# Kernel tuning notes

Hardware: AMD Instinct MI355X
Metric: run time of the kernel (lower is better)

The kernel has to match this reference:

```python
import jax, jax.numpy as jnp
import numpy as np
import math

B, S, D, H, DFF, E, TOPK = 2, 2048, 768, 12, 3072, 8, 2
DH = D // H
EPS = 1e-5


def _ln(x, g, b):
    mu = jnp.mean(x, axis=-1, keepdims=True)
    var = jnp.mean(jnp.square(x - mu), axis=-1, keepdims=True)
    return (x - mu) * jax.lax.rsqrt(var + EPS) * g + b


def _router(x, rw, rb):
    # x: [B,S,D] -> probs [B,S,E], topk indices [B,S,K]
    logits = jnp.einsum('bsd,de->bse', x, rw) + rb
    probs = jax.nn.softmax(logits, axis=-1)
    topv, topi = jax.lax.top_k(probs, TOPK)
    return probs, topv, topi


def setup_inputs() -> dict:
    key = jax.random.key(0)
    ks = jax.random.split(key, 12)
    s = 0.02
    inp = {
        'x': jax.random.normal(ks[0], (B, S, D), dtype=jnp.float32),
        'wq': jax.random.normal(ks[1], (D, D), dtype=jnp.float32) * s,
        'bq': jnp.zeros((D,), jnp.float32),
        'wk': jax.random.normal(ks[2], (D, D), dtype=jnp.float32) * s,
        'bk': jnp.zeros((D,), jnp.float32),
        'wv': jax.random.normal(ks[3], (D, D), dtype=jnp.float32) * s,
        'bv': jnp.zeros((D,), jnp.float32),
        'wo': jax.random.normal(ks[4], (D, D), dtype=jnp.float32) * s,
        'bo': jnp.zeros((D,), jnp.float32),
        'norm1_g': jnp.ones((D,), jnp.float32),
        'norm1_b': jnp.zeros((D,), jnp.float32),
        'router_w': jax.random.normal(ks[5], (D, E), dtype=jnp.float32) * s,
        'router_b': jnp.zeros((E,), jnp.float32),
        'ew1': jax.random.normal(ks[6], (E, D, DFF), dtype=jnp.float32) * s,
        'eb1': jnp.zeros((E, DFF), jnp.float32),
        'ew2': jax.random.normal(ks[7], (E, DFF, D), dtype=jnp.float32) * s,
        'eb2': jnp.zeros((E, D), jnp.float32),
        'norm2_g': jnp.ones((D,), jnp.float32),
        'norm2_b': jnp.zeros((D,), jnp.float32),
    }
    return inp


def reference(x, wq, bq, wk, bk, wv, bv, wo, bo,
              norm1_g, norm1_b, router_w, router_b,
              ew1, eb1, ew2, eb2, norm2_g, norm2_b):
    # ---- multi-head self-attention ----
    def proj(w, b):
        return (jnp.einsum('bsd,de->bse', x, w) + b).reshape(B, S, H, DH).transpose(0, 2, 1, 3)
    q, k, v = proj(wq, bq), proj(wk, bk), proj(wv, bv)
    scores = jnp.einsum('bhqd,bhkd->bhqk', q, k) / math.sqrt(DH)
    attn = jax.nn.softmax(scores, axis=-1)
    ctx = jnp.einsum('bhqk,bhkd->bhqd', attn, v).transpose(0, 2, 1, 3).reshape(B, S, D)
    attn_out = jnp.einsum('bsd,de->bse', ctx, wo) + bo
    x1 = _ln(x + attn_out, norm1_g, norm1_b)

    # ---- MoE: top-k routing with renormalized gates ----
    probs, topv, topi = _router(x1, router_w, router_b)
    gates = topv / jnp.sum(topv, axis=-1, keepdims=True)          # [B,S,K]
    # combine weights per expert: [B,S,E]
    combine = jnp.sum(jax.nn.one_hot(topi, E, dtype=x1.dtype) * gates[..., None], axis=-2)
    moe_out = jnp.zeros_like(x1)
    for e in range(E):  # fixed small expert count
        h = jax.nn.relu(jnp.einsum('bsd,df->bsf', x1, ew1[e]) + eb1[e])
        y = jnp.einsum('bsf,fd->bsd', h, ew2[e]) + eb2[e]
        moe_out = moe_out + combine[..., e:e + 1] * y
    x2 = _ln(x1 + moe_out, norm2_g, norm2_b)

    # ---- redundant second router call + load-balancing aux loss ----
    probs2, _, topi2 = _router(x2, router_w, router_b)
    mask2 = jax.nn.one_hot(topi2, E, dtype=x2.dtype)              # [B,S,K,E]
    frac = jnp.mean(mask2, axis=(0, 1, 2))                        # fraction routed per expert
    prob = jnp.mean(probs2, axis=(0, 1))                          # mean router prob per expert
    aux_loss = E * jnp.sum(frac * prob)
    return (x2, aux_loss)
```

## Files before the change

kernel.cpp:

```cpp
#include <hip/hip_runtime.h>

typedef _Float16 f16;
typedef _Float16 f16x8 __attribute__((ext_vector_type(8)));
typedef _Float16 f16x4v __attribute__((ext_vector_type(4)));
typedef float f32x4 __attribute__((ext_vector_type(4)));

#define THREADS 256
#define BM 128
#define BN 128
#define BKK 64

#define WSCALE 256.0f
#define WDESCALE (1.0f/256.0f)

static __device__ __forceinline__ float wred_sum(float x){
#pragma unroll
  for (int o = 32; o; o >>= 1) x += __shfl_xor(x, o);
  return x;
}
static __device__ __forceinline__ int wred_sumi(int x){
#pragma unroll
  for (int o = 32; o; o >>= 1) x += __shfl_xor(x, o);
  return x;
}
static __device__ __forceinline__ float bred_sum(float x){
  __shared__ float r[4];
  x = wred_sum(x);
  if ((threadIdx.x & 63) == 0) r[threadIdx.x >> 6] = x;
  __syncthreads();
  float s = r[0] + r[1] + r[2] + r[3];
  __syncthreads();
  return s;
}

template<class Epi>
static __device__ __forceinline__ void gemm_core(const f16* A, const f16* BT,
                                                 int m0, int K, int N, int n0, Epi epi)
{
  __shared__ __align__(16) f16 Al[BM][BKK];
  __shared__ __align__(16) f16 Bl[BN][BKK];
  const int t = threadIdx.x;
  const int lane = t & 63, wave = t >> 6;
  const int wr = wave >> 1, wc = wave & 1;

  const f16* gA[4];
  const f16* gB[4];
#pragma unroll
  for (int i = 0; i < 4; ++i) {
    int c = i * THREADS + t;
    int r = c >> 3;
    int kc = (((c & 7) ^ (r & 7)) << 3);
    gA[i] = A + (size_t)(m0 + r) * K + kc;
    gB[i] = BT + (size_t)(n0 + r) * K + kc;
  }

  f32x4 acc[4][4];
#pragma unroll
  for (int i = 0; i < 4; ++i)
#pragma unroll
    for (int j = 0; j < 4; ++j)
#pragma unroll
      for (int r = 0; r < 4; ++r) acc[i][j][r] = 0.0f;

  f16* Als = &Al[0][0];
  f16* Bls = &Bl[0][0];

  for (int k0 = 0; k0 < K; k0 += BKK) {
    __syncthreads();
#pragma unroll
    for (int i = 0; i < 4; ++i) {
      int c = i * THREADS + t;
      __builtin_amdgcn_global_load_lds(
          (const __attribute__((address_space(1))) void*)(gA[i] + k0),
          (__attribute__((address_space(3))) void*)(Als + (size_t)c * 8), 16, 0, 0);
      __builtin_amdgcn_global_load_lds(
          (const __attribute__((address_space(1))) void*)(gB[i] + k0),
          (__attribute__((address_space(3))) void*)(Bls + (size_t)c * 8), 16, 0, 0);
    }
    __syncthreads();
#pragma unroll
    for (int kk = 0; kk < BKK; kk += 32) {
      const int lrow = lane & 15, lk = (lane >> 4) * 8;
      const int sx = (lrow & 7) << 3;
      f16x8 af[4], bf[4];
#pragma unroll
      for (int mf = 0; mf < 4; ++mf)
        af[mf] = *(const f16x8*)&Als[(size_t)(wr * 64 + mf * 16 + lrow) * BKK + ((kk + lk) ^ sx)];
#pragma unroll
      for (int nf = 0; nf < 4; ++nf)
        bf[nf] = *(const f16x8*)&Bls[(size_t)(wc * 64 + nf * 16 + lrow) * BKK + ((kk + lk) ^ sx)];
#pragma unroll
      for (int mf = 0; mf < 4; ++mf)
#pragma unroll
        for (int nf = 0; nf < 4; ++nf)
          acc[mf][nf] = __builtin_amdgcn_mfma_f32_16x16x32_f16(af[mf], bf[nf], acc[mf][nf], 0, 0, 0);
    }
  }
  const int lr4 = (lane >> 4) * 4, lc = lane & 15;
#pragma unroll
  for (int mf = 0; mf < 4; ++mf)
#pragma unroll
    for (int nf = 0; nf < 4; ++nf)
#pragma unroll
      for (int r = 0; r < 4; ++r) {
        int row = wr * 64 + mf * 16 + lr4 + r;
        int col = n0 + wc * 64 + nf * 16 + lc;
        epi(row, col, acc[mf][nf][r]);
      }
}

__global__ __launch_bounds__(256) void k_cvt(const float* x, f16* o){
  size_t i = (size_t)blockIdx.x * 256 + threadIdx.x;
  float4 v = ((const float4*)x)[i];
  f16x4v h;
  h[0] = (f16)v.x; h[1] = (f16)v.y; h[2] = (f16)v.z; h[3] = (f16)v.w;
  *(f16x4v*)(o + i * 4) = h;
}

__global__ __launch_bounds__(256) void k_transpose(const float* in, f16* out, int Kd, int Nd){
  __shared__ float tl[32][33];
  const float* ip = in + (size_t)blockIdx.z * Kd * Nd;
  f16* op = out + (size_t)blockIdx.z * Kd * Nd;
  int n0 = blockIdx.x * 32, k0 = blockIdx.y * 32;
  int tx = threadIdx.x & 31, ty = threadIdx.x >> 5;
#pragma unroll
  for (int j = 0; j < 32; j += 8) tl[ty + j][tx] = ip[(size_t)(k0 + ty + j) * Nd + n0 + tx];
  __syncthreads();
#pragma unroll
  for (int j = 0; j < 32; j += 8) op[(size_t)(n0 + ty + j) * Kd + k0 + tx] = (f16)(tl[tx][ty + j] * WSCALE);
}

__global__ __launch_bounds__(256) void k_gemm_qkv(const f16* xb,
    const f16* wqT, const f16* wkT, const f16* wvT,
    const float* bq, const float* bk, const float* bv,
    f16* Q, f16* Ko, f16* V)
{
  int m0 = blockIdx.x * 128, n0 = blockIdx.y * 128, z = blockIdx.z;
  const f16* BT = (z == 0) ? wqT : ((z == 1) ? wkT : wvT);
  const float* bias = (z == 0) ? bq : ((z == 1) ? bk : bv);
  auto epi = [&](int row, int col, float vv) {
    int grow = m0 + row;
    int b = grow >> 11, s = grow & 2047;
    int h = col >> 6, dh = col & 63;
    float val = vv * WDESCALE + bias[col];
    if (z == 2) V[(((size_t)b * 12 + h) * 64 + dh) * 2048 + s] = (f16)val;
    else ((z == 0) ? Q : Ko)[(((size_t)b * 12 + h) * 2048 + s) * 64 + dh] = (f16)val;
  };
  gemm_core(xb, BT, m0, 768, 768, n0, epi);
}

__global__ __launch_bounds__(256, 4) void k_fattn(const f16* Qf, const f16* Kf,
                                                  const f16* Vf, float* Opart, float* lpart)
{
  __shared__ __align__(16) f16 Kl[64][72];
  __shared__ __align__(16) f16 Vl[64][72];
  __shared__ __align__(16) f16 Pl[64][72];
  const int t = threadIdx.x, lane = t & 63, wid = t >> 6;
  const int lc = lane & 15, g = lane >> 4;
  const int q0 = blockIdx.x * 64, bh = blockIdx.y, sp = blockIdx.z;
  const f16* Qh = Qf + (size_t)bh * 2048 * 64;
  const f16* Kh = Kf + ((size_t)bh * 2048 + sp * 1024) * 64;
  const f16* Vh = Vf + (size_t)bh * 64 * 2048 + sp * 1024;

  const float C1 = 0.125f * 1.44269504f;
  const float C2 = 9.0f - 2.0f * 1.44269504f;

  f16x8 aq[2];
#pragma unroll
  for (int kk = 0; kk < 2; ++kk)
    aq[kk] = *(const f16x8*)(Qh + (size_t)(q0 + wid * 16 + lc) * 64 + kk * 32 + g * 8);

  f32x4 acco[4];
  float l_[4];
#pragma unroll
  for (int nf = 0; nf < 4; ++nf)
#pragma unroll
    for (int r = 0; r < 4; ++r) acco[nf][r] = 0.f;
#pragma unroll
  for (int r = 0; r < 4; ++r) l_[r] = 0.f;

  f16x8 sk[2], sv[2];
#pragma unroll
  for (int i = 0; i < 2; ++i) {
    int c = i * 256 + t;
    sk[i] = *(const f16x8*)(Kh + (size_t)(c >> 3) * 64 + (c & 7) * 8);
    sv[i] = *(const f16x8*)(Vh + (size_t)(c >> 3) * 2048 + (c & 7) * 8);
  }

  for (int j = 0; j < 16; ++j) {
    __syncthreads();
#pragma unroll
    for (int i = 0; i < 2; ++i) {
      int c = i * 256 + t;
      *(f16x8*)&Kl[c >> 3][(c & 7) * 8] = sk[i];
      *(f16x8*)&Vl[c >> 3][(c & 7) * 8] = sv[i];
    }
    __syncthreads();

    if (j < 15) {
      const int kv1 = (j + 1) * 64;
#pragma unroll
      for (int i = 0; i < 2; ++i) {
        int c = i * 256 + t;
        sk[i] = *(const f16x8*)(Kh + (size_t)(kv1 + (c >> 3)) * 64 + (c & 7) * 8);
        sv[i] = *(const f16x8*)(Vh + (size_t)(c >> 3) * 2048 + kv1 + (c & 7) * 8);
      }
    }

    f32x4 acc[4];
#pragma unroll
    for (int nf = 0; nf < 4; ++nf)
#pragma unroll
      for (int r = 0; r < 4; ++r) acc[nf][r] = 0.f;
#pragma unroll
    for (int kk = 0; kk < 2; ++kk) {
      f16x8 bk[4];
#pragma unroll
      for (int nf = 0; nf < 4; ++nf) bk[nf] = *(const f16x8*)&Kl[nf * 16 + lc][kk * 32 + g * 8];
#pragma unroll
      for (int nf = 0; nf < 4; ++nf)
        acc[nf] = __builtin_amdgcn_mfma_f32_16x16x32_f16(aq[kk], bk[nf], acc[nf], 0, 0, 0);
    }

    {
      const int prow = wid * 16 + g * 4;
#pragma unroll
      for (int r = 0; r < 4; ++r) {
        float ls = 0.f;
#pragma unroll
        for (int nf = 0; nf < 4; ++nf) {
          float p = exp2f(fmaf(acc[nf][r], C1, C2));
          Pl[prow + r][nf * 16 + lc] = (f16)p;
          ls += p;
        }
        l_[r] += ls;
      }
    }

#pragma unroll
    for (int kk = 0; kk < 2; ++kk) {
      f16x8 ap, bv[4];
      ap = *(const f16x8*)&Pl[wid * 16 + lc][kk * 32 + g * 8];
#pragma unroll
      for (int nf = 0; nf < 4; ++nf) bv[nf] = *(const f16x8*)&Vl[nf * 16 + lc][kk * 32 + g * 8];
#pragma unroll
      for (int nf = 0; nf < 4; ++nf)
        acco[nf] = __builtin_amdgcn_mfma_f32_16x16x32_f16(ap, bv[nf], acco[nf], 0, 0, 0);
    }
  }

  float* Op = Opart + ((size_t)(sp * 24 + bh) * 2048 + q0) * 64;
  float* lp = lpart + (size_t)(sp * 24 + bh) * 2048 + q0;
#pragma unroll
  for (int r = 0; r < 4; ++r) {
    float lr = l_[r];
#pragma unroll
    for (int o = 1; o < 16; o <<= 1) lr += __shfl_xor(lr, o);
    if (lc == 0) lp[wid * 16 + g * 4 + r] = lr;
#pragma unroll
    for (int nf = 0; nf < 4; ++nf)
      Op[(size_t)(wid * 16 + g * 4 + r) * 64 + nf * 16 + lc] = acco[nf][r];
  }
}

__global__ __launch_bounds__(256) void k_attcomb(const float* Opart, const float* lpart, f16* ctx){
  size_t base = ((size_t)blockIdx.x * 256 + threadIdx.x) * 4;
  size_t row = base >> 6; int dh = base & 63;
  int bh = (int)(row >> 11), qr = (int)(row & 2047);
  int b = bh / 12, h = bh - b * 12;
  const float4 o0 = *(const float4*)(Opart + base);
  const float4 o1 = *(const float4*)(Opart + base + (size_t)24 * 2048 * 64);
  float inv = 1.f / (lpart[row] + lpart[row + 24 * 2048]);
  f16x4v hv;
  hv[0] = (f16)((o0.x + o1.x) * inv);
  hv[1] = (f16)((o0.y + o1.y) * inv);
  hv[2] = (f16)((o0.z + o1.z) * inv);
  hv[3] = (f16)((o0.w + o1.w) * inv);
  *(f16x4v*)(ctx + ((size_t)b * 2048 + qr) * 768 + h * 64 + dh) = hv;
}

__global__ __launch_bounds__(256) void k_gemm_oproj(const f16* ctx, const f16* woT,
    const float* bo, const float* x, float* x1pre)
{
  int m0 = blockIdx.x * 128, n0 = blockIdx.y * 128;
  auto epi = [&](int row, int col, float vv) {
    size_t i = (size_t)(m0 + row) * 768 + col;
    x1pre[i] = x[i] + vv * WDESCALE + bo[col];
  };
  gemm_core(ctx, woT, m0, 768, 768, n0, epi);
}

__global__ __launch_bounds__(256) void k_ln(const float* in, const float* add,
    const float* g, const float* b, float* outf, f16* outh)
{
  size_t row = blockIdx.x;
  int t = threadIdx.x;
  const float* p = in + row * 768;
  float v[3];
  float s = 0.f;
#pragma unroll
  for (int i = 0; i < 3; ++i) {
    float xv = p[t + i * 256];
    if (add) xv += add[row * 768 + t + i * 256];
    v[i] = xv; s += xv;
  }
  float mu = bred_sum(s) * (1.f / 768.f);
  float q = 0.f;
#pragma unroll
  for (int i = 0; i < 3; ++i) { float d = v[i] - mu; q += d * d; }
  float var = bred_sum(q) * (1.f / 768.f);
  float inv = rsqrtf(var + 1e-5f);
#pragma unroll
  for (int i = 0; i < 3; ++i) {
    int c = t + i * 256;
    float y = (v[i] - mu) * inv * g[c] + b[c];
    outf[row * 768 + c] = y;
    if (outh) outh[row * 768 + c] = (f16)y;
  }
}

__global__ __launch_bounds__(256) void k_ln_moe(const float* x1, const f16* ys,
    const int* inv_map, const float* gates, const float* g, const float* b, float* outf)
{
  size_t row = blockIdx.x;
  int t = threadIdx.x;
  int sl0 = inv_map[row * 2], sl1 = inv_map[row * 2 + 1];
  float g0 = gates[row * 2], g1 = gates[row * 2 + 1];
  const float* p = x1 + row * 768;
  const f16* y0 = ys + (size_t)sl0 * 768;
  const f16* y1 = ys + (size_t)sl1 * 768;
  float v[3];
  float s = 0.f;
#pragma unroll
  for (int i = 0; i < 3; ++i) {
    int c = t + i * 256;
    float xv = p[c] + g0 * (float)y0[c] + g1 * (float)y1[c];
    v[i] = xv; s += xv;
  }
  float mu = bred_sum(s) * (1.f / 768.f);
  float q = 0.f;
#pragma unroll
  for (int i = 0; i < 3; ++i) { float d = v[i] - mu; q += d * d; }
  float var = bred_sum(q) * (1.f / 768.f);
  float inv = rsqrtf(var + 1e-5f);
#pragma unroll
  for (int i = 0; i < 3; ++i) {
    int c = t + i * 256;
    outf[row * 768 + c] = (v[i] - mu) * inv * g[c] + b[c];
  }
}

__global__ __launch_bounds__(256) void k_router(const float* X, const float* rw, const float* rb,
    int* topi, float* gates, float* pprob_part, int* pcnt_part, int mode)
{
  __shared__ float sp[4][8];
  __shared__ int   si[4][2];
  int wave = threadIdx.x >> 6;
  int tok = blockIdx.x * 4 + wave;
  int lane = threadIdx.x & 63;
  const float* xr = X + (size_t)tok * 768;
  float a0=0,a1=0,a2=0,a3=0,a4=0,a5=0,a6=0,a7=0;
#pragma unroll
  for (int i = 0; i < 12; ++i) {
    int d = lane + i * 64;
    float xv = xr[d];
    float4 w0 = *(const float4*)(rw + d * 8);
    float4 w1 = *(const float4*)(rw + d * 8 + 4);
    a0 += xv*w0.x; a1 += xv*w0.y; a2 += xv*w0.z; a3 += xv*w0.w;
    a4 += xv*w1.x; a5 += xv*w1.y; a6 += xv*w1.z; a7 += xv*w1.w;
  }
  a0=wred_sum(a0); a1=wred_sum(a1); a2=wred_sum(a2); a3=wred_sum(a3);
  a4=wred_sum(a4); a5=wred_sum(a5); a6=wred_sum(a6); a7=wred_sum(a7);
  if (lane == 0) {
    float lg[8] = {a0+rb[0],a1+rb[1],a2+rb[2],a3+rb[3],a4+rb[4],a5+rb[5],a6+rb[6],a7+rb[7]};
    float mx = lg[0];
    for (int e = 1; e < 8; ++e) mx = fmaxf(mx, lg[e]);
    float pp[8], ssum = 0.f;
    for (int e = 0; e < 8; ++e) { pp[e] = expf(lg[e] - mx); ssum += pp[e]; }
    float invs = 1.f / ssum;
    for (int e = 0; e < 8; ++e) pp[e] *= invs;
    int i1 = 0; float p1 = pp[0];
    for (int e = 1; e < 8; ++e) if (pp[e] > p1) { p1 = pp[e]; i1 = e; }
    int i2 = -1; float p2 = -1.f;
    for (int e = 0; e < 8; ++e) if (e != i1 && pp[e] > p2) { p2 = pp[e]; i2 = e; }
    if (mode == 1) {
      float gs = 1.f / (p1 + p2);
      topi[tok*2] = i1; topi[tok*2+1] = i2;
      gates[tok*2] = p1*gs; gates[tok*2+1] = p2*gs;
    } else {
      for (int e = 0; e < 8; ++e) sp[wave][e] = pp[e];
      si[wave][0] = i1; si[wave][1] = i2;
    }
  }
  if (mode == 2) {
    __syncthreads();
    int t = threadIdx.x;
    if (t < 8) {
      float s = sp[0][t] + sp[1][t] + sp[2][t] + sp[3][t];
      int c = 0;
#pragma unroll
      for (int w = 0; w < 4; ++w) c += (si[w][0] == t) + (si[w][1] == t);
      pprob_part[blockIdx.x * 8 + t] = s;
      pcnt_part[blockIdx.x * 8 + t] = c;
    }
  }
}

__global__ __launch_bounds__(256) void k_plan(const int* topi, int* offal, int* tile_e, int* tile_r0){
  __shared__ int hist[8];
  int t = threadIdx.x, lane = t & 63;
  if (t < 8) hist[t] = 0;
  __syncthreads();
  int loc[8] = {0,0,0,0,0,0,0,0};
  for (int i = t; i < 8192; i += 256) ++loc[topi[i]];
#pragma unroll
  for (int e = 0; e < 8; ++e) {
    int s = wred_sumi(loc[e]);
    if (lane == 0) atomicAdd(&hist[e], s);
  }
  __syncthreads();
  if (t == 0) {
    int off = 0, tt = 0;
    for (int e = 0; e < 8; ++e) {
      offal[e] = off;
      int nt = (hist[e] + 127) >> 7;
      for (int i = 0; i < nt; ++i) { tile_e[tt] = e; tile_r0[tt] = off + i * 128; ++tt; }
      off += nt << 7;
    }
    for (; tt < 80; ++tt) { tile_e[tt] = -1; tile_r0[tt] = 0; }
  }
}

__global__ __launch_bounds__(512) void k_scatter(const int* topi, const float* gates,
    const int* offal, int* perm, float* gate_s, int* inv_map)
{
  int w = threadIdx.x >> 6, lane = threadIdx.x & 63;
  int base = offal[w];
  for (int it = 0; it < 128; ++it) {
    int i = it * 64 + lane;
    int e = topi[i];
    bool act = (e == w);
    unsigned long long mask = __ballot(act);
    if (act) {
      int pos = base + __popcll(mask & ((1ull << lane) - 1ull));
      perm[pos] = i >> 1;
      gate_s[pos] = gates[i];
      inv_map[i] = pos;
    }
    base += __popcll(mask);
  }
}

__global__ __launch_bounds__(256) void k_gather(const f16* x1b, const int* perm, f16* xg){
  size_t i = (size_t)blockIdx.x * 256 + threadIdx.x;
  int row = (int)(i / 96), col8 = (int)(i % 96);
  int src = perm[row];
  *(f16x8*)(xg + (size_t)row * 768 + col8 * 8) =
      *(const f16x8*)(x1b + (size_t)src * 768 + col8 * 8);
}

__global__ __launch_bounds__(256) void k_gemm_moe1(const f16* xg, const f16* ew1T,
    const float* eb1, const int* tile_e, const int* tile_r0, f16* hbuf)
{
  int e = tile_e[blockIdx.x];
  if (e < 0) return;
  int s0 = tile_r0[blockIdx.x];
  int n0 = blockIdx.y * 128;
  const f16* BT = ew1T + (size_t)e * 3072 * 768;
  const float* be = eb1 + e * 3072;
  auto epi = [&](int row, int col, float vv) {
    hbuf[(size_t)(s0 + row) * 3072 + col] = (f16)fmaxf(vv * WDESCALE + be[col], 0.f);
  };
  gemm_core(xg + (size_t)s0 * 768, BT, 0, 768, 3072, n0, epi);
}

__global__ __launch_bounds__(256) void k_gemm_moe2(const f16* hbuf, const f16* ew2T,
    const float* eb2, const int* tile_e, const int* tile_r0, f16* yslots)
{
  int e = tile_e[blockIdx.x];
  if (e < 0) return;
  int s0 = tile_r0[blockIdx.x];
  int n0 = blockIdx.y * 128;
  const f16* A = hbuf + (size_t)s0 * 3072;
  const f16* BT = ew2T + (size_t)e * 768 * 3072;
  const float* be = eb2 + e * 768;
  auto epi = [&](int row, int col, float vv) {
    yslots[(size_t)(s0 + row) * 768 + col] = (f16)(vv * WDESCALE + be[col]);
  };
  gemm_core(A, BT, 0, 3072, 768, n0, epi);
}

__global__ __launch_bounds__(256) void k_final(const float* pprob, const int* pcnt, float* out){
  __shared__ float sp[256];
  __shared__ int sc[256];
  int t = threadIdx.x, e = t & 7, g = t >> 3;
  float s = 0.f; int c = 0;
  for (int b = g; b < 1024; b += 32) { s += pprob[b * 8 + e]; c += pcnt[b * 8 + e]; }
  sp[t] = s; sc[t] = c;
  __syncthreads();
  if (t < 8) {
    float ss = 0.f; int cc = 0;
    for (int g2 = 0; g2 < 32; ++g2) { ss += sp[t + g2 * 8]; cc += sc[t + g2 * 8]; }
    sp[t] = ss; sc[t] = cc;
  }
  __syncthreads();
  if (t == 0) {
    float a = 0.f;
    for (int e2 = 0; e2 < 8; ++e2)
      a += ((float)sc[e2] * (1.f / 8192.f)) * (sp[e2] * (1.f / 4096.f));
    out[(size_t)4096 * 768] = 8.f * a;
  }
}

extern "C" void kernel_launch(void* const* d_in, const int* in_sizes, int n_in,
                              void* d_out, int out_size, void* d_ws, size_t ws_size,
                              hipStream_t stream)
{
  const float* x   = (const float*)d_in[0];
  const float* wq  = (const float*)d_in[1];
  const float* bq  = (const float*)d_in[2];
  const float* wk  = (const float*)d_in[3];
  const float* bk  = (const float*)d_in[4];
  const float* wv  = (const float*)d_in[5];
  const float* bv  = (const float*)d_in[6];
  const float* wo  = (const float*)d_in[7];
  const float* bo  = (const float*)d_in[8];
  const float* n1g = (const float*)d_in[9];
  const float* n1b = (const float*)d_in[10];
  const float* rw  = (const float*)d_in[11];
  const float* rb  = (const float*)d_in[12];
  const float* ew1 = (const float*)d_in[13];
  const float* eb1 = (const float*)d_in[14];
  const float* ew2 = (const float*)d_in[15];
  const float* eb2 = (const float*)d_in[16];
  const float* n2g = (const float*)d_in[17];
  const float* n2b = (const float*)d_in[18];
  float* out = (float*)d_out;
  char* ws = (char*)d_ws;

  size_t oWQT,oWKT,oWVT,oWOT,oEW1T,oEW2T,oXB,oQ,oK,oV,oCTX,oX1,oX1B,oYS;
  size_t oTOPI,oGATES,oOFF,oTE,oTR,oPERM,oGS,oINV,oXG,oH,oPP,oPC,oOP,oLP;

  {
    size_t off = 0;
    auto al = [&](size_t bytes) { size_t o = off; off += (bytes + 255) & ~(size_t)255; return o; };
    oWQT = al((size_t)768*768*2); oWKT = al((size_t)768*768*2);
    oWVT = al((size_t)768*768*2); oWOT = al((size_t)768*768*2);
    oEW1T = al((size_t)8*768*3072*2); oEW2T = al((size_t)8*768*3072*2);
    oXB  = al((size_t)4096*768*2);
    oQ   = al((size_t)24*2048*64*2); oK = al((size_t)24*2048*64*2); oV = al((size_t)24*2048*64*2);
    oCTX = al((size_t)4096*768*2);
    oX1  = al((size_t)4096*768*4);
    oX1B = al((size_t)4096*768*2);
    oYS  = al((size_t)9216*768*2);
    oTOPI = al(4096*2*4); oGATES = al(4096*2*4);
    oOFF = al(256);
    oTE = al(512); oTR = al(512);
    oPERM = al(9216*4); oGS = al(9216*4); oINV = al(8192*4);
    oXG = al((size_t)9216*768*2);
    oH = al((size_t)9216*3072*2);
    oPP = al(1024*8*4); oPC = al(1024*8*4);
    oOP = al((size_t)2*24*2048*64*4);
    oLP = al((size_t)2*24*2048*4);
    (void)ws_size;
  }

  f16* wqT  = (f16*)(ws + oWQT);
  f16* wkT  = (f16*)(ws + oWKT);
  f16* wvT  = (f16*)(ws + oWVT);
  f16* woT  = (f16*)(ws + oWOT);
  f16* ew1T = (f16*)(ws + oEW1T);
  f16* ew2T = (f16*)(ws + oEW2T);
  f16* xb   = (f16*)(ws + oXB);
  f16* Qf   = (f16*)(ws + oQ);
  f16* Kf   = (f16*)(ws + oK);
  f16* Vf   = (f16*)(ws + oV);
  f16* ctxb = (f16*)(ws + oCTX);
  float* x1 = (float*)(ws + oX1);
  f16* x1bb = (f16*)(ws + oX1B);
  f16* yslots = (f16*)(ws + oYS);
  int* topi = (int*)(ws + oTOPI);
  float* gates = (float*)(ws + oGATES);
  int* offal  = (int*)(ws + oOFF);
  int* tile_e = (int*)(ws + oTE);
  int* tile_r0= (int*)(ws + oTR);
  int* perm   = (int*)(ws + oPERM);
  float* gate_s = (float*)(ws + oGS);
  int* inv_map = (int*)(ws + oINV);
  f16* xg     = (f16*)(ws + oXG);
  f16* hbuf   = (f16*)(ws + oH);
  float* pprob = (float*)(ws + oPP);
  int* pcnt   = (int*)(ws + oPC);
  float* Opart = (float*)(ws + oOP);
  float* lpart = (float*)(ws + oLP);

  (void)in_sizes; (void)n_in; (void)out_size;

  hipMemsetAsync(ws + oPERM, 0, 2 * 9216 * 4, stream);

  k_cvt<<<3072, 256, 0, stream>>>(x, xb);
  k_transpose<<<dim3(24,24,1), 256, 0, stream>>>(wq, wqT, 768, 768);
  k_transpose<<<dim3(24,24,1), 256, 0, stream>>>(wk, wkT, 768, 768);
  k_transpose<<<dim3(24,24,1), 256, 0, stream>>>(wv, wvT, 768, 768);
  k_transpose<<<dim3(24,24,1), 256, 0, stream>>>(wo, woT, 768, 768);
  k_transpose<<<dim3(96,24,8), 256, 0, stream>>>(ew1, ew1T, 768, 3072);
  k_transpose<<<dim3(24,96,8), 256, 0, stream>>>(ew2, ew2T, 3072, 768);

  k_gemm_qkv<<<dim3(32,6,3), 256, 0, stream>>>(xb, wqT, wkT, wvT, bq, bk, bv, Qf, Kf, Vf);
  k_fattn<<<dim3(32,24,2), 256, 0, stream>>>(Qf, Kf, Vf, Opart, lpart);
  k_attcomb<<<3072, 256, 0, stream>>>(Opart, lpart, ctxb);
  k_gemm_oproj<<<dim3(32,6), 256, 0, stream>>>(ctxb, woT, bo, x, x1);
  k_ln<<<4096, 256, 0, stream>>>(x1, nullptr, n1g, n1b, x1, x1bb);

  k_router<<<1024, 256, 0, stream>>>(x1, rw, rb, topi, gates, pprob, pcnt, 1);
  k_plan<<<1, 256, 0, stream>>>(topi, offal, tile_e, tile_r0);
  k_scatter<<<1, 512, 0, stream>>>(topi, gates, offal, perm, gate_s, inv_map);
  k_gather<<<3456, 256, 0, stream>>>(x1bb, perm, xg);
  k_gemm_moe1<<<dim3(72,24), 256, 0, stream>>>(xg, ew1T, eb1, tile_e, tile_r0, hbuf);
  k_gemm_moe2<<<dim3(72,6), 256, 0, stream>>>(hbuf, ew2T, eb2, tile_e, tile_r0, yslots);

  k_ln_moe<<<4096, 256, 0, stream>>>(x1, yslots, inv_map, gates, n2g, n2b, out);
  k_router<<<1024, 256, 0, stream>>>(out, rw, rb, topi, gates, pprob, pcnt, 2);
  k_final<<<1, 256, 0, stream>>>(pprob, pcnt, out);
}
```

Before: 453.7 us.

## Use 256x256 double-buffered MFMA tiles for MoE up-projection GEMM

Replaces the shared 128x128 GEMM core in the first MoE GEMM with a dedicated 512-thread kernel. It computes 256x256 output tiles, double-buffers them in LDS filled by direct global-to-LDS loads with an XOR swizzle, and uses 16x16x32 f16 MFMAs. The aim is more operand reuse per byte loaded and fewer blocks. Expert segments are now padded to 256 rows, so the planner emits separate 128-row tile lists for the second GEMM and the buffers grow. This adds wasted work on padded rows in both GEMMs, and the large LDS footprint limits occupancy.

```diff
diff --git a/kernel.cpp b/kernel.cpp
--- a/kernel.cpp
+++ b/kernel.cpp
@@ -406,7 +406,9 @@
   }
 }
 
-__global__ __launch_bounds__(256) void k_plan(const int* topi, int* offal, int* tile_e, int* tile_r0){
+__global__ __launch_bounds__(256) void k_plan(const int* topi, int* offal,
+    int* tile_e, int* tile_r0, int* tile_e2, int* tile_r02)
+{
   __shared__ int hist[8];
   int t = threadIdx.x, lane = t & 63;
   if (t < 8) hist[t] = 0;
@@ -420,14 +422,19 @@
   }
   __syncthreads();
   if (t == 0) {
-    int off = 0, tt = 0;
+    int off = 0, t1 = 0, t2 = 0;
     for (int e = 0; e < 8; ++e) {
       offal[e] = off;
-      int nt = (hist[e] + 127) >> 7;
-      for (int i = 0; i < nt; ++i) { tile_e[tt] = e; tile_r0[tt] = off + i * 128; ++tt; }
-      off += nt << 7;
-    }
-    for (; tt < 80; ++tt) { tile_e[tt] = -1; tile_r0[tt] = 0; }
+      int nt = (hist[e] + 255) >> 8;
+      for (int i = 0; i < nt; ++i) {
+        tile_e[t1] = e; tile_r0[t1] = off + i * 256; ++t1;
+        tile_e2[t2] = e; tile_r02[t2] = off + i * 256; ++t2;
+        tile_e2[t2] = e; tile_r02[t2] = off + i * 256 + 128; ++t2;
+      }
+      off += nt << 8;
+    }
+    for (; t1 < 40; ++t1) { tile_e[t1] = -1; tile_r0[t1] = 0; }
+    for (; t2 < 80; ++t2) { tile_e2[t2] = -1; tile_r02[t2] = 0; }
   }
 }
 
@@ -459,27 +466,105 @@
       *(const f16x8*)(x1b + (size_t)src * 768 + col8 * 8);
 }
 
-__global__ __launch_bounds__(256) void k_gemm_moe1(const f16* xg, const f16* ew1T,
+__global__ __launch_bounds__(512, 2) void k_gemm_moe1(const f16* xg, const f16* ew1T,
     const float* eb1, const int* tile_e, const int* tile_r0, f16* hbuf)
 {
+  __shared__ __align__(16) f16 Al[2][256][64];
+  __shared__ __align__(16) f16 Bl[2][256][64];
   int e = tile_e[blockIdx.x];
   if (e < 0) return;
   int s0 = tile_r0[blockIdx.x];
-  int n0 = blockIdx.y * 128;
-  const f16* BT = ew1T + (size_t)e * 3072 * 768;
+  int n0 = blockIdx.y * 256;
+  const f16* A  = xg + (size_t)s0 * 768;
+  const f16* BT = ew1T + (size_t)e * 3072 * 768 + (size_t)n0 * 768;
   const float* be = eb1 + e * 3072;
-  auto epi = [&](int row, int col, float vv) {
-    hbuf[(size_t)(s0 + row) * 3072 + col] = (f16)fmaxf(vv * WDESCALE + be[col], 0.f);
+
+  const int t = threadIdx.x;
+  const int lane = t & 63, wave = t >> 6;
+  const int wr = wave >> 2, wc = wave & 3;
+
+  const f16* gA[4];
+  const f16* gB[4];
+#pragma unroll
+  for (int i = 0; i < 4; ++i) {
+    int c = i * 512 + t;
+    int r = c >> 3;
+    int kc = (((c & 7) ^ (r & 7)) << 3);
+    gA[i] = A + (size_t)r * 768 + kc;
+    gB[i] = BT + (size_t)r * 768 + kc;
+  }
+
+  f32x4 acc[8][4];
+#pragma unroll
+  for (int i = 0; i < 8; ++i)
+#pragma unroll
+    for (int j = 0; j < 4; ++j)
+#pragma unroll
+      for (int r = 0; r < 4; ++r) acc[i][j][r] = 0.0f;
+
+  auto stage = [&](int buf, int k0) {
+    f16* Ad = &Al[buf][0][0];
+    f16* Bd = &Bl[buf][0][0];
+#pragma unroll
+    for (int i = 0; i < 4; ++i) {
+      int c = i * 512 + t;
+      __builtin_amdgcn_global_load_lds(
+          (const __attribute__((address_space(1))) void*)(gA[i] + k0),
+          (__attribute__((address_space(3))) void*)(Ad + (size_t)c * 8), 16, 0, 0);
+      __builtin_amdgcn_global_load_lds(
+          (const __attribute__((address_space(1))) void*)(gB[i] + k0),
+          (__attribute__((address_space(3))) void*)(Bd + (size_t)c * 8), 16, 0, 0);
+    }
   };
-  gemm_core(xg + (size_t)s0 * 768, BT, 0, 768, 3072, n0, epi);
+
+  stage(0, 0);
+  __syncthreads();
+
+  int cur = 0;
+  for (int ks = 0; ks < 12; ++ks) {
+    if (ks < 11) stage(cur ^ 1, (ks + 1) * 64);
+    const f16* Ab = &Al[cur][0][0];
+    const f16* Bb = &Bl[cur][0][0];
+#pragma unroll
+    for (int kk = 0; kk < 64; kk += 32) {
+      const int lrow = lane & 15, lk = (lane >> 4) * 8;
+      const int sx = (lrow & 7) << 3;
+      f16x8 af[8], bf[4];
+#pragma unroll
+      for (int mf = 0; mf < 8; ++mf)
+        af[mf] = *(const f16x8*)&Ab[(size_t)(wr * 128 + mf * 16 + lrow) * 64 + ((kk + lk) ^ sx)];
+#pragma unroll
+      for (int nf = 0; nf < 4; ++nf)
+        bf[nf] = *(const f16x8*)&Bb[(size_t)(wc * 64 + nf * 16 + lrow) * 64 + ((kk + lk) ^ sx)];
+#pragma unroll
+      for (int mf = 0; mf < 8; ++mf)
+#pragma unroll
+        for (int nf = 0; nf < 4; ++nf)
+          acc[mf][nf] = __builtin_amdgcn_mfma_f32_16x16x32_f16(af[mf], bf[nf], acc[mf][nf], 0, 0, 0);
+    }
+    __syncthreads();
+    cur ^= 1;
+  }
+
+  const int lr4 = (lane >> 4) * 4, lc = lane & 15;
+#pragma unroll
+  for (int mf = 0; mf < 8; ++mf)
+#pragma unroll
+    for (int nf = 0; nf < 4; ++nf)
+#pragma unroll
+      for (int r = 0; r < 4; ++r) {
+        int row = wr * 128 + mf * 16 + lr4 + r;
+        int col = n0 + wc * 64 + nf * 16 + lc;
+        hbuf[(size_t)(s0 + row) * 3072 + col] = (f16)fmaxf(acc[mf][nf][r] * WDESCALE + be[col], 0.f);
+      }
 }
 
 __global__ __launch_bounds__(256) void k_gemm_moe2(const f16* hbuf, const f16* ew2T,
-    const float* eb2, const int* tile_e, const int* tile_r0, f16* yslots)
-{
-  int e = tile_e[blockIdx.x];
+    const float* eb2, const int* tile_e2, const int* tile_r02, f16* yslots)
+{
+  int e = tile_e2[blockIdx.x];
   if (e < 0) return;
-  int s0 = tile_r0[blockIdx.x];
+  int s0 = tile_r02[blockIdx.x];
   int n0 = blockIdx.y * 128;
   const f16* A = hbuf + (size_t)s0 * 3072;
   const f16* BT = ew2T + (size_t)e * 768 * 3072;
@@ -539,7 +624,7 @@
   char* ws = (char*)d_ws;
 
   size_t oWQT,oWKT,oWVT,oWOT,oEW1T,oEW2T,oXB,oQ,oK,oV,oCTX,oX1,oX1B,oYS;
-  size_t oTOPI,oGATES,oOFF,oTE,oTR,oPERM,oGS,oINV,oXG,oH,oPP,oPC,oOP,oLP;
+  size_t oTOPI,oGATES,oOFF,oTE,oTR,oTE2,oTR2,oPERM,oGS,oINV,oXG,oH,oPP,oPC,oOP,oLP;
 
   {
     size_t off = 0;
@@ -552,13 +637,13 @@
     oCTX = al((size_t)4096*768*2);
     oX1  = al((size_t)4096*768*4);
     oX1B = al((size_t)4096*768*2);
-    oYS  = al((size_t)9216*768*2);
+    oYS  = al((size_t)10240*768*2);
     oTOPI = al(4096*2*4); oGATES = al(4096*2*4);
     oOFF = al(256);
-    oTE = al(512); oTR = al(512);
-    oPERM = al(9216*4); oGS = al(9216*4); oINV = al(8192*4);
-    oXG = al((size_t)9216*768*2);
-    oH = al((size_t)9216*3072*2);
+    oTE = al(256); oTR = al(256); oTE2 = al(512); oTR2 = al(512);
+    oPERM = al(10240*4); oGS = al(10240*4); oINV = al(8192*4);
+    oXG = al((size_t)10240*768*2);
+    oH = al((size_t)10240*3072*2);
     oPP = al(1024*8*4); oPC = al(1024*8*4);
     oOP = al((size_t)2*24*2048*64*4);
     oLP = al((size_t)2*24*2048*4);
@@ -584,6 +669,8 @@
   int* offal  = (int*)(ws + oOFF);
   int* tile_e = (int*)(ws + oTE);
   int* tile_r0= (int*)(ws + oTR);
+  int* tile_e2 = (int*)(ws + oTE2);
+  int* tile_r02= (int*)(ws + oTR2);
   int* perm   = (int*)(ws + oPERM);
   float* gate_s = (float*)(ws + oGS);
   int* inv_map = (int*)(ws + oINV);
@@ -596,7 +683,7 @@
 
   (void)in_sizes; (void)n_in; (void)out_size;
 
-  hipMemsetAsync(ws + oPERM, 0, 2 * 9216 * 4, stream);
+  hipMemsetAsync(ws + oPERM, 0, 2 * 10240 * 4, stream);
 
   k_cvt<<<3072, 256, 0, stream>>>(x, xb);
   k_transpose<<<dim3(24,24,1), 256, 0, stream>>>(wq, wqT, 768, 768);
@@ -613,11 +700,11 @@
   k_ln<<<4096, 256, 0, stream>>>(x1, nullptr, n1g, n1b, x1, x1bb);
 
   k_router<<<1024, 256, 0, stream>>>(x1, rw, rb, topi, gates, pprob, pcnt, 1);
-  k_plan<<<1, 256, 0, stream>>>(topi, offal, tile_e, tile_r0);
+  k_plan<<<1, 256, 0, stream>>>(topi, offal, tile_e, tile_r0, tile_e2, tile_r02);
   k_scatter<<<1, 512, 0, stream>>>(topi, gates, offal, perm, gate_s, inv_map);
-  k_gather<<<3456, 256, 0, stream>>>(x1bb, perm, xg);
-  k_gemm_moe1<<<dim3(72,24), 256, 0, stream>>>(xg, ew1T, eb1, tile_e, tile_r0, hbuf);
-  k_gemm_moe2<<<dim3(72,6), 256, 0, stream>>>(hbuf, ew2T, eb2, tile_e, tile_r0, yslots);
+  k_gather<<<3840, 256, 0, stream>>>(x1bb, perm, xg);
+  k_gemm_moe1<<<dim3(40,12), 512, 0, stream>>>(xg, ew1T, eb1, tile_e, tile_r0, hbuf);
+  k_gemm_moe2<<<dim3(80,6), 256, 0, stream>>>(hbuf, ew2T, eb2, tile_e2, tile_r02, yslots);
 
   k_ln_moe<<<4096, 256, 0, stream>>>(x1, yslots, inv_map, gates, n2g, n2b, out);
   k_router<<<1024, 256, 0, stream>>>(out, rw, rb, topi, gates, pprob, pcnt, 2);
```

After: 457.0 us. Within noise of the previous version (+0.7%).
